# Kernel optimization log

Hardware: AMD Instinct MI355X
Metric: run time of the kernel (lower is better)

The kernel has to match this reference:

```python
import jax, jax.numpy as jnp
import numpy as np

BATCH = 4096
DIM = 128
TEMPERATURE = 0.1


def setup_inputs() -> dict:
    key = jax.random.key(0)
    k1, k2 = jax.random.split(key)
    out1 = jax.random.normal(k1, (BATCH, DIM), dtype=jnp.float32)
    out2 = jax.random.normal(k2, (BATCH, DIM), dtype=jnp.float32)
    return {"out1": out1, "out2": out2}


def reference(out1, out2):
    B = out1.shape[0]
    total = jnp.concatenate([out1, out2], axis=0)                 # [2B, D]
    total = total / jnp.linalg.norm(total, axis=1, keepdims=True)  # L2 normalize rows
    sim = jnp.matmul(total, total.T) / TEMPERATURE                 # [2B, 2B]
    # mask the diagonal with -1e9 (matches masked_fill_ with float('-1e9'))
    diag_mask = jnp.eye(2 * B, dtype=bool)
    sim = jnp.where(diag_mask, jnp.float32(-1e9), sim)
    log_prob = -jax.nn.log_softmax(sim, axis=1)                    # [2B, 2B]
    # vectorized positive-pair diagonal gather: (k, B+k) and (B+k, k)
    idx = jnp.arange(B)
    pos = log_prob[idx, idx + B] + log_prob[idx + B, idx]          # [B]
    loss = jnp.sum(pos)
    # faithful to original: loss / 2 * batch_size == (loss / 2) * B
    return loss / 2 * B
```

## Files before the change

### kernel.cpp

```cpp
#include <hip/hip_runtime.h>
#include <hip/hip_bf16.h>
#include <cstdint>


typedef __bf16 bf16x8 __attribute__((ext_vector_type(8)));
typedef __bf16 bf16x2 __attribute__((ext_vector_type(2)));
typedef float  f32x4  __attribute__((ext_vector_type(4)));

#define NROWS 8192
#define DIM   128
#define ALPHA 3.7982827f
#define LN2   0.6931471805599453f

__device__ __forceinline__ void load_lds16(const void* g, void* l) {
    __builtin_amdgcn_global_load_lds(
        (const __attribute__((address_space(1))) unsigned int*)(uintptr_t)g,
        (__attribute__((address_space(3))) unsigned int*)(uintptr_t)l,
        16, 0, 0);
}


__global__ __launch_bounds__(256) void norm_kernel(
    const float* __restrict__ out1, const float* __restrict__ out2,
    __bf16* __restrict__ nb, float* __restrict__ rowsum, float* __restrict__ dout)
{
    const int t = threadIdx.x, lane = t & 63, wid = t >> 6;
    const int row = blockIdx.x * 4 + wid;
    const float* src = (row < 4096) ? (out1 + (size_t)row * DIM)
                                    : (out2 + (size_t)(row - 4096) * DIM);
    float2 v = ((const float2*)src)[lane];
    float ss = v.x * v.x + v.y * v.y;
    #pragma unroll
    for (int off = 1; off < 64; off <<= 1) ss += __shfl_xor(ss, off);
    const float s = rsqrtf(ss) * ALPHA;

    const int c  = lane >> 2;
    const int cs = (c & 8) | ((c ^ row) & 7);
    const int idx = row * DIM + cs * 8 + ((2 * lane) & 7);
    bf16x2 w;
    w.x = (__bf16)(v.x * s);
    w.y = (__bf16)(v.y * s);
    *(bf16x2*)(nb + idx) = w;

    if (blockIdx.x < 32) rowsum[blockIdx.x * 256 + t] = 0.0f;
    if (blockIdx.x == 0 && t == 0) dout[0] = 0.0f;
}

__global__ __launch_bounds__(256, 2) void simloss_main(
    const __bf16* __restrict__ nb, float* __restrict__ rowsum)
{
    __shared__ __bf16 Bsm[128 * DIM];
    const int t = threadIdx.x, lane = t & 63, wid = t >> 6;
    const int quad = lane >> 4, l15 = lane & 15;
    const int rb = blockIdx.x, cb = blockIdx.y;
    const int rowbase = rb * 128 + (wid & 1) * 64;
    const int ncol0   = (wid >> 1) * 64;

    int cso[4];
    #pragma unroll
    for (int k = 0; k < 4; ++k) {
        int c = k * 4 + quad;
        cso[k] = ((c & 8) | ((c ^ lane) & 7)) * 8;
    }

    bf16x8 afrag[4][4];
    #pragma unroll
    for (int mt = 0; mt < 4; ++mt) {
        const __bf16* ar = nb + (size_t)(rowbase + mt * 16 + l15) * DIM;
        #pragma unroll
        for (int k = 0; k < 4; ++k) afrag[mt][k] = *(const bf16x8*)(ar + cso[k]);
    }

    float rowpart[4][4] = {};

    for (int ct = 0; ct < 8; ++ct) {
        __syncthreads();
        const char* gB = (const char*)(nb + (size_t)(cb * 1024 + ct * 128) * DIM);
        char* lB = (char*)Bsm + wid * 1024;
        const char* gBw = gB + wid * 1024 + lane * 16;
        #pragma unroll
        for (int i = 0; i < 8; ++i) load_lds16(gBw + i * 4096, lB + i * 4096);
        __syncthreads();

        f32x4 acc[4][4] = {};
        #pragma unroll
        for (int k = 0; k < 4; ++k) {
            bf16x8 b[4];
            #pragma unroll
            for (int nt = 0; nt < 4; ++nt)
                b[nt] = *(const bf16x8*)(Bsm + (ncol0 + nt * 16 + l15) * DIM + cso[k]);
            #pragma unroll
            for (int mt = 0; mt < 4; ++mt)
                #pragma unroll
                for (int nt = 0; nt < 4; ++nt)
                    acc[mt][nt] = __builtin_amdgcn_mfma_f32_16x16x32_bf16(
                        afrag[mt][k], b[nt], acc[mt][nt], 0, 0, 0);
        }

        #pragma unroll
        for (int mt = 0; mt < 4; ++mt)
            #pragma unroll
            for (int nt = 0; nt < 4; ++nt)
                #pragma unroll
                for (int r = 0; r < 4; ++r)
                    rowpart[mt][r] += __builtin_amdgcn_exp2f(acc[mt][nt][r]);
    }

    #pragma unroll
    for (int mt = 0; mt < 4; ++mt)
        #pragma unroll
        for (int r = 0; r < 4; ++r) {
            float v = rowpart[mt][r];
            v += __shfl_xor(v, 1);
            v += __shfl_xor(v, 2);
            v += __shfl_xor(v, 4);
            v += __shfl_xor(v, 8);
            if (l15 == 0)
                atomicAdd(&rowsum[rowbase + mt * 16 + quad * 4 + r], v);
        }
}

__global__ __launch_bounds__(256) void finalize_kernel(
    const __bf16* __restrict__ nb, const float* __restrict__ rowsum,
    float* __restrict__ dout)
{
    const int t = threadIdx.x, lane = t & 63, wid = t >> 6;
    const int w = blockIdx.x * 4 + wid;
    float wacc = 0.0f;
    for (int rr = 0; rr < 16; ++rr) {
        const int i = w * 16 + rr;
        const int p = i ^ 4096;
        bf16x2 av = *(const bf16x2*)(nb + (size_t)i * DIM + 2 * lane);
        bf16x2 bv = *(const bf16x2*)(nb + (size_t)p * DIM + 2 * lane);
        float ax = (float)av.x, ay = (float)av.y;
        float bx = (float)bv.x, by = (float)bv.y;
        float self = ax * ax + ay * ay;
        float pos  = ax * bx + ay * by;
        #pragma unroll
        for (int off = 1; off < 64; off <<= 1) {
            self += __shfl_xor(self, off);
            pos  += __shfl_xor(pos, off);
        }
        if (lane == 0) {
            float se = rowsum[i] - __builtin_amdgcn_exp2f(self);
            wacc += logf(se) - pos * LN2;
        }
    }
    if (lane == 0) atomicAdd(dout, wacc * 2048.0f);
}

extern "C" void kernel_launch(void* const* d_in, const int* in_sizes, int n_in,
                              void* d_out, int out_size, void* d_ws, size_t ws_size,
                              hipStream_t stream)
{
    const float* out1 = (const float*)d_in[0];
    const float* out2 = (const float*)d_in[1];
    __bf16* nb     = (__bf16*)d_ws;
    float*  rowsum = (float*)((char*)d_ws + (size_t)NROWS * DIM * 2);
    float*  dout   = (float*)d_out;

    hipLaunchKernelGGL(norm_kernel, dim3(2048), dim3(256), 0, stream,
                       out1, out2, nb, rowsum, dout);
    hipLaunchKernelGGL(simloss_main, dim3(64, 8), dim3(256), 0, stream,
                       (const __bf16*)nb, rowsum);
    hipLaunchKernelGGL(finalize_kernel, dim3(128), dim3(256), 0, stream,
                       (const __bf16*)nb, rowsum, dout);
}
```

Before: 91.89 us.

## Exploit symmetry of similarity matrix with triangular block enumeration

```diff
diff --git a/kernel.cpp b/kernel.cpp
--- a/kernel.cpp
+++ b/kernel.cpp
@@ -49,12 +49,23 @@
 __global__ __launch_bounds__(256, 2) void simloss_main(
     const __bf16* __restrict__ nb, float* __restrict__ rowsum)
 {
-    __shared__ __bf16 Bsm[128 * DIM];
+    __shared__ __bf16 Bsm[2][128 * DIM];
+    __shared__ float colpart[256];
+
     const int t = threadIdx.x, lane = t & 63, wid = t >> 6;
     const int quad = lane >> 4, l15 = lane & 15;
-    const int rb = blockIdx.x, cb = blockIdx.y;
+
+    const int b = (int)blockIdx.x;
+    int cb = (int)(0.5f * (sqrtf(4.0f * (float)b + 1.0f) - 1.0f));
+    if (cb < 0) cb = 0;
+    while (cb > 0 && cb * (cb + 1) > b) --cb;
+    while ((cb + 1) * (cb + 2) <= b) ++cb;
+    const int rb = b - cb * (cb + 1);
+    const int above = (rb < 2 * cb);
+
     const int rowbase = rb * 128 + (wid & 1) * 64;
     const int ncol0   = (wid >> 1) * 64;
+    const int colblk  = cb * 256;
 
     int cso[4];
     #pragma unroll
@@ -63,6 +74,16 @@
         cso[k] = ((c & 8) | ((c ^ lane) & 7)) * 8;
     }
 
+    {
+        const char* gB  = (const char*)(nb + (size_t)colblk * DIM);
+        char*       lB  = (char*)(&Bsm[0][0]) + wid * 1024;
+        const char* gBw = gB + wid * 1024 + lane * 16;
+        #pragma unroll
+        for (int i = 0; i < 8; ++i) load_lds16(gBw + i * 4096, lB + i * 4096);
+    }
+
+    colpart[t] = 0.0f;
+
     bf16x8 afrag[4][4];
     #pragma unroll
     for (int mt = 0; mt < 4; ++mt) {
@@ -73,38 +94,63 @@
 
     float rowpart[4][4] = {};
 
-    for (int ct = 0; ct < 8; ++ct) {
-        __syncthreads();
-        const char* gB = (const char*)(nb + (size_t)(cb * 1024 + ct * 128) * DIM);
-        char* lB = (char*)Bsm + wid * 1024;
+    __syncthreads();
+
+    {
+        const char* gB  = (const char*)(nb + (size_t)(colblk + 128) * DIM);
+        char*       lB  = (char*)(&Bsm[1][0]) + wid * 1024;
         const char* gBw = gB + wid * 1024 + lane * 16;
         #pragma unroll
         for (int i = 0; i < 8; ++i) load_lds16(gBw + i * 4096, lB + i * 4096);
-        __syncthreads();
-
+    }
+
+    #pragma unroll
+    for (int ct = 0; ct < 2; ++ct) {
+        const __bf16* Bs = &Bsm[ct][0];
         f32x4 acc[4][4] = {};
         #pragma unroll
         for (int k = 0; k < 4; ++k) {
-            bf16x8 b[4];
+            bf16x8 bfr[4];
             #pragma unroll
             for (int nt = 0; nt < 4; ++nt)
-                b[nt] = *(const bf16x8*)(Bsm + (ncol0 + nt * 16 + l15) * DIM + cso[k]);
+                bfr[nt] = *(const bf16x8*)(Bs + (ncol0 + nt * 16 + l15) * DIM + cso[k]);
             #pragma unroll
             for (int mt = 0; mt < 4; ++mt)
                 #pragma unroll
                 for (int nt = 0; nt < 4; ++nt)
                     acc[mt][nt] = __builtin_amdgcn_mfma_f32_16x16x32_bf16(
-                        afrag[mt][k], b[nt], acc[mt][nt], 0, 0, 0);
-        }
-
+                        afrag[mt][k], bfr[nt], acc[mt][nt], 0, 0, 0);
+        }
+
+        float csum[4] = {};
         #pragma unroll
         for (int mt = 0; mt < 4; ++mt)
             #pragma unroll
-            for (int nt = 0; nt < 4; ++nt)
+            for (int nt = 0; nt < 4; ++nt) {
+                float cs = 0.0f;
                 #pragma unroll
-                for (int r = 0; r < 4; ++r)
-                    rowpart[mt][r] += __builtin_amdgcn_exp2f(acc[mt][nt][r]);
-    }
+                for (int r = 0; r < 4; ++r) {
+                    float e = __builtin_amdgcn_exp2f(acc[mt][nt][r]);
+                    rowpart[mt][r] += e;
+                    cs += e;
+                }
+                csum[nt] += cs;
+            }
+
+        if (above) {
+            #pragma unroll
+            for (int nt = 0; nt < 4; ++nt) {
+                float v = csum[nt];
+                v += __shfl_xor(v, 16);
+                v += __shfl_xor(v, 32);
+                if (quad == 0)
+                    atomicAdd(&colpart[ct * 128 + ncol0 + nt * 16 + l15], v);
+            }
+        }
+        if (ct == 0) __syncthreads();
+    }
+
+    __syncthreads();
 
     #pragma unroll
     for (int mt = 0; mt < 4; ++mt)
@@ -118,6 +164,9 @@
             if (l15 == 0)
                 atomicAdd(&rowsum[rowbase + mt * 16 + quad * 4 + r], v);
         }
+
+    if (above)
+        atomicAdd(&rowsum[colblk + t], colpart[t]);
 }
 
 __global__ __launch_bounds__(256) void finalize_kernel(
@@ -127,8 +176,9 @@
     const int t = threadIdx.x, lane = t & 63, wid = t >> 6;
     const int w = blockIdx.x * 4 + wid;
     float wacc = 0.0f;
-    for (int rr = 0; rr < 16; ++rr) {
-        const int i = w * 16 + rr;
+    #pragma unroll
+    for (int rr = 0; rr < 4; ++rr) {
+        const int i = w * 4 + rr;
         const int p = i ^ 4096;
         bf16x2 av = *(const bf16x2*)(nb + (size_t)i * DIM + 2 * lane);
         bf16x2 bv = *(const bf16x2*)(nb + (size_t)p * DIM + 2 * lane);
@@ -161,8 +211,8 @@
 
     hipLaunchKernelGGL(norm_kernel, dim3(2048), dim3(256), 0, stream,
                        out1, out2, nb, rowsum, dout);
-    hipLaunchKernelGGL(simloss_main, dim3(64, 8), dim3(256), 0, stream,
+    hipLaunchKernelGGL(simloss_main, dim3(1056), dim3(256), 0, stream,
                        (const __bf16*)nb, rowsum);
-    hipLaunchKernelGGL(finalize_kernel, dim3(128), dim3(256), 0, stream,
+    hipLaunchKernelGGL(finalize_kernel, dim3(512), dim3(256), 0, stream,
                        (const __bf16*)nb, rowsum, dout);
 }
```

Result: slower. 112.6 us (+22.5%).
